# Kernel tuning notes

Hardware: AMD Instinct MI355X
Metric: run time of the kernel (lower is better)

Reference implementation:

```python
import jax, jax.numpy as jnp
import numpy as np

B, N, CIN, H, OUT, L, K = 8, 512, 64, 64, 64, 256, 3
EPS = 1e-5


def setup_inputs() -> dict:
    key = jax.random.key(0)
    ks = jax.random.split(key, 12)
    def unif(k, shape, fan):
        s = 1.0 / np.sqrt(fan)
        return jax.random.uniform(k, shape, jnp.float32, -s, s)
    return {
        "x": jax.random.normal(ks[0], (B, N, CIN, L), jnp.float32),
        "adj": jax.random.uniform(ks[1], (B, N, N), jnp.float32),
        # temp_conv1: Conv1d(CIN->H, k=3)
        "w1": unif(ks[2], (H, CIN, K), CIN * K),
        "b1": unif(ks[3], (H,), CIN * K),
        # graph_conv: Linear-style (H,H) + bias, stdv=1/sqrt(out_features)
        "gw": unif(ks[4], (H, H), H),
        "gb": unif(ks[5], (H,), H),
        # temp_conv2: Conv1d(H->OUT, k=3)
        "w2": unif(ks[6], (OUT, H, K), H * K),
        "b2": unif(ks[7], (OUT,), H * K),
        # residual: Conv1d(CIN->OUT, k=1) == pointwise linear
        "wr": unif(ks[8], (OUT, CIN), CIN),
        "br": unif(ks[9], (OUT,), CIN),
        # BatchNorm2d(OUT) affine params
        "gamma": jnp.ones((OUT,), jnp.float32),
        "beta": jnp.zeros((OUT,), jnp.float32),
    }


def _conv1d(x, w, b, pad):
    # x: (B, N, C, L) -> flatten node dim into batch, NCH conv
    b_, n_, c, l = x.shape
    y = jax.lax.conv_general_dilated(
        x.reshape(b_ * n_, c, l), w, window_strides=(1,),
        padding=[(pad, pad)], dimension_numbers=("NCH", "OIH", "NCH"))
    y = y + b[None, :, None]
    return y.reshape(b_, n_, w.shape[0], l)


def reference(x, adj, w1, b1, gw, gb, w2, b2, wr, br, gamma, beta):
    pad = (K - 1) // 2
    # residual branch: 1x1 conv over channels
    residual = jnp.einsum("bncl,oc->bnol", x, wr) + br[None, None, :, None]
    # temporal conv 1
    out = _conv1d(x, w1, b1, pad)                      # (B,N,H,L)
    # graph conv over all timesteps at once (replaces per-t Python loop)
    xw = jnp.einsum("bnhl,hd->bndl", out, gw)          # (B,N,H,L)
    out = jnp.einsum("bnm,bmdl->bndl", adj, xw) + gb[None, None, :, None]
    # temporal conv 2
    out = _conv1d(out, w2, b2, pad)                    # (B,N,OUT,L)
    out = out + residual
    # BatchNorm2d over channel axis (training-mode batch stats, biased var)
    mean = jnp.mean(out, axis=(0, 1, 3), keepdims=True)
    var = jnp.mean(jnp.square(out - mean), axis=(0, 1, 3), keepdims=True)
    out = (out - mean) * jax.lax.rsqrt(var + EPS)
    out = out * gamma[None, None, :, None] + beta[None, None, :, None]
    return jax.nn.relu(out)
```

## Files before the change

### kernel.cpp

```cpp
#include <hip/hip_runtime.h>
#include <hip/hip_bf16.h>
#include <stdint.h>


typedef unsigned short u16;
typedef unsigned int   u32;
typedef __attribute__((ext_vector_type(8))) short           bf16x8;
typedef __attribute__((ext_vector_type(8))) unsigned short  u16x8;
typedef __attribute__((ext_vector_type(4))) unsigned short  u16x4;
typedef __attribute__((ext_vector_type(4))) float           f32x4;

__device__ __forceinline__ float bf2f(u16 v){
  union { u32 u; float f; } x; x.u = ((u32)v) << 16; return x.f;
}
__device__ __forceinline__ u16 f2bf(float f){
  __hip_bfloat16 h = __float2bfloat16(f);
  return *reinterpret_cast<u16*>(&h);
}
__device__ __forceinline__ u32 swz(int row, int cbyte){
  return (u32)(row * 128) + (u32)(cbyte ^ ((row & 7) << 4));
}

__global__ __launch_bounds__(256) void k_prep(const float* __restrict__ w1, const float* __restrict__ b1,
    const float* __restrict__ gw, const float* __restrict__ w2, const float* __restrict__ wr,
    u16* __restrict__ w1g, float* __restrict__ b1g, u16* __restrict__ w2t, u16* __restrict__ wrt){
  const int gt = blockIdx.x * 256 + threadIdx.x, gs = gridDim.x * 256;
  for (int e = gt; e < 12288; e += gs){
    int tap = e >> 12, rem = e & 4095, o = rem >> 6, c = rem & 63;
    w2t[e] = f2bf(w2[(o * 64 + c) * 3 + tap]);
    float s = 0.f;
    for (int h = 0; h < 64; ++h)
      s += gw[h * 64 + o] * w1[(h * 64 + c) * 3 + tap];
    w1g[e] = f2bf(s);
  }
  for (int e = gt; e < 4096; e += gs) wrt[e] = f2bf(wr[e]);
  for (int d = gt; d < 64; d += gs){
    float s = 0.f;
    for (int h = 0; h < 64; ++h) s += b1[h] * gw[h * 64 + d];
    b1g[d] = s;
  }
}

__global__ __launch_bounds__(256) void k_p1(const float* __restrict__ x,
    const u16* __restrict__ w1g, const float* __restrict__ b1g,
    const u16* __restrict__ wrt, u16* __restrict__ outA, u16* __restrict__ outR){
  __shared__ u16 tile[16384];
  const int t = threadIdx.x;
  const size_t bn = (size_t)blockIdx.x + (size_t)blockIdx.y * 512;
  const float* xb = x + bn * 16384;

  {
    const int c0 = (t >> 3) * 2;
    #pragma unroll
    for (int v = 0; v < 8; ++v){
      const int l0 = (t & 7) * 4 + v * 32;
      f32x4 a = *(const f32x4*)(xb + (size_t)c0 * 256 + l0);
      f32x4 b = *(const f32x4*)(xb + (size_t)(c0 + 1) * 256 + l0);
      #pragma unroll
      for (int e = 0; e < 4; ++e){
        u32 p = (u32)f2bf(a[e]) | ((u32)f2bf(b[e]) << 16);
        *(u32*)((char*)tile + swz(l0 + e, c0 * 2)) = p;
      }
    }
  }
  __syncthreads();
  const int w = t >> 6, ln = t & 63, lq = ln >> 4, lr = ln & 15;
  const bf16x8 z8 = {};

  {
    f32x4 racc[4][4];
    #pragma unroll
    for (int i = 0; i < 4; ++i)
      #pragma unroll
      for (int j = 0; j < 4; ++j) racc[i][j] = (f32x4){0.f, 0.f, 0.f, 0.f};
    #pragma unroll
    for (int kk = 0; kk < 2; ++kk){
      bf16x8 A[4];
      #pragma unroll
      for (int fo = 0; fo < 4; ++fo)
        A[fo] = *(const bf16x8*)(wrt + (fo * 16 + lr) * 64 + kk * 32 + lq * 8);
      #pragma unroll
      for (int fc = 0; fc < 4; ++fc){
        int l = w * 64 + fc * 16 + lr;
        bf16x8 B = *(const bf16x8*)((char*)tile + swz(l, kk * 64 + lq * 16));
        #pragma unroll
        for (int fo = 0; fo < 4; ++fo)
          racc[fo][fc] = __builtin_amdgcn_mfma_f32_16x16x32_bf16(A[fo], B, racc[fo][fc], 0, 0, 0);
      }
    }
    #pragma unroll
    for (int v = 0; v < 8; ++v){
      u16x8 ov;
      const int fo = v >> 1;
      #pragma unroll
      for (int h = 0; h < 2; ++h){
        const int fc = (v & 1) * 2 + h;
        #pragma unroll
        for (int r2 = 0; r2 < 4; ++r2)
          ov[h * 4 + r2] = f2bf(racc[fo][fc][r2]);
      }
      *(u16x8*)(outR + bn * 16384 + v * 2048 + t * 8) = ov;
    }
  }

  f32x4 acc[4][4];
  #pragma unroll
  for (int i = 0; i < 4; ++i)
    #pragma unroll
    for (int j = 0; j < 4; ++j) acc[i][j] = (f32x4){0.f, 0.f, 0.f, 0.f};
  #pragma unroll
  for (int tap = 0; tap < 3; ++tap){
    #pragma unroll
    for (int kk = 0; kk < 2; ++kk){
      bf16x8 A[4];
      #pragma unroll
      for (int fo = 0; fo < 4; ++fo)
        A[fo] = *(const bf16x8*)(w1g + tap * 4096 + (fo * 16 + lr) * 64 + kk * 32 + lq * 8);
      #pragma unroll
      for (int fc = 0; fc < 4; ++fc){
        int r = w * 64 + fc * 16 + lr + tap - 1;
        int rc = r < 0 ? 0 : (r > 255 ? 255 : r);
        bf16x8 B = *(const bf16x8*)((char*)tile + swz(rc, kk * 64 + lq * 16));
        if (r != rc) B = z8;
        #pragma unroll
        for (int fo = 0; fo < 4; ++fo)
          acc[fo][fc] = __builtin_amdgcn_mfma_f32_16x16x32_bf16(A[fo], B, acc[fo][fc], 0, 0, 0);
      }
    }
  }
  __syncthreads();
  #pragma unroll
  for (int fo = 0; fo < 4; ++fo){
    float bb[4];
    #pragma unroll
    for (int r2 = 0; r2 < 4; ++r2) bb[r2] = b1g[fo * 16 + lq * 4 + r2];
    #pragma unroll
    for (int fc = 0; fc < 4; ++fc){
      int l = w * 64 + fc * 16 + lr;
      #pragma unroll
      for (int r2 = 0; r2 < 4; ++r2){
        int d = fo * 16 + lq * 4 + r2;
        *(u16*)((char*)tile + l * 128 + ((2 * d) ^ ((l & 7) << 4))) = f2bf(acc[fo][fc][r2] + bb[r2]);
      }
    }
  }
  __syncthreads();
  u16* op = outA + bn * 16384;
  #pragma unroll
  for (int v = 0; v < 8; ++v){
    int flat = v * 2048 + t * 8;
    int l = flat >> 6, d0 = flat & 63;
    u16x8 val = *(const u16x8*)((char*)tile + l * 128 + ((d0 * 2) ^ ((l & 7) << 4)));
    *(u16x8*)(op + flat) = val;
  }
}

__global__ __launch_bounds__(256) void k_p3(const u16* __restrict__ xw,
    const float* __restrict__ adj, const float* __restrict__ gbv, u16* __restrict__ outB){
  __shared__ u16 At[8192];
  __shared__ u16 Bt[8192];
  const int t = threadIdx.x;
  const int wg = ((blockIdx.x & 7) << 9) | ((int)blockIdx.x >> 3);
  const int jt = wg & 127, nt = (wg >> 7) & 3, b = wg >> 9;
  const float* adjb = adj + ((size_t)b * 512 + (size_t)nt * 128) * 512;
  const u16* Xb = xw + (size_t)b * 8388608 + (size_t)jt * 128;
  const int w = t >> 6, ln = t & 63, lq = ln >> 4, lr = ln & 15;
  const int wrow = w >> 1, wcol = w & 1;
  const int mpair = t & 31, jq = t >> 5;
  f32x4 acc[4][4];
  #pragma unroll
  for (int i = 0; i < 4; ++i)
    #pragma unroll
    for (int j = 0; j < 4; ++j) acc[i][j] = (f32x4){0.f, 0.f, 0.f, 0.f};

  f32x4 ra[8];
  u16x8 rb[4];
  auto LOADK = [&](int ks){
    #pragma unroll
    for (int it = 0; it < 8; ++it){
      int c = it * 256 + t;
      int row = c >> 4, mc = c & 15;
      ra[it] = *(const f32x4*)(adjb + (size_t)row * 512 + ks * 64 + mc * 4);
    }
    const u16* s0 = Xb + (size_t)(ks * 64 + mpair * 2) * 16384 + jq * 16;
    const u16* s1 = s0 + 16384;
    #pragma unroll
    for (int v2 = 0; v2 < 2; ++v2){
      rb[v2 * 2]     = *(const u16x8*)(s0 + v2 * 8);
      rb[v2 * 2 + 1] = *(const u16x8*)(s1 + v2 * 8);
    }
  };

  LOADK(0);
  for (int ks = 0; ks < 8; ++ks){
    #pragma unroll
    for (int it = 0; it < 8; ++it){
      int c = it * 256 + t;
      int row = c >> 4, mc = c & 15;
      u16x4 pk;
      #pragma unroll
      for (int e = 0; e < 4; ++e) pk[e] = f2bf(ra[it][e]);
      *(u16x4*)((char*)At + (u32)(row * 128) + (u32)((mc * 8) ^ ((row & 7) << 4))) = pk;
    }
    #pragma unroll
    for (int v2 = 0; v2 < 2; ++v2){
      #pragma unroll
      for (int e = 0; e < 8; ++e){
        u32 p = (u32)(u16)rb[v2 * 2][e] | ((u32)(u16)rb[v2 * 2 + 1][e] << 16);
        *(u32*)((char*)Bt + swz(jq * 16 + v2 * 8 + e, mpair * 4)) = p;
      }
    }
    __syncthreads();
    if (ks < 7) LOADK(ks + 1);
    #pragma unroll
    for (int kk = 0; kk < 2; ++kk){
      bf16x8 Af[4], Bf[4];
      #pragma unroll
      for (int f = 0; f < 4; ++f){
        int rA = wrow * 64 + f * 16 + lr;
        Af[f] = *(const bf16x8*)((char*)At + swz(rA, kk * 64 + lq * 16));
        int rB = wcol * 64 + f * 16 + lr;
        Bf[f] = *(const bf16x8*)((char*)Bt + swz(rB, kk * 64 + lq * 16));
      }
      #pragma unroll
      for (int fr = 0; fr < 4; ++fr)
        #pragma unroll
        for (int fc = 0; fc < 4; ++fc)
          acc[fr][fc] = __builtin_amdgcn_mfma_f32_16x16x32_bf16(Af[fr], Bf[fc], acc[fr][fc], 0, 0, 0);
    }
    __syncthreads();
  }
  float gbl[4];
  #pragma unroll
  for (int fc = 0; fc < 4; ++fc) gbl[fc] = gbv[fc * 16 + lr];
  u16* ob = outB + ((size_t)b * 512 + (size_t)nt * 128) * 16384 + (size_t)jt * 128;
  #pragma unroll
  for (int fr = 0; fr < 4; ++fr)
    #pragma unroll
    for (int fc = 0; fc < 4; ++fc)
      #pragma unroll
      for (int r2 = 0; r2 < 4; ++r2){
        int n_ = wrow * 64 + fr * 16 + lq * 4 + r2;
        int j_ = wcol * 64 + fc * 16 + lr;
        ob[(size_t)n_ * 16384 + j_] = f2bf(acc[fr][fc][r2] + gbl[fc]);
      }
}

__global__ __launch_bounds__(256) void k_p4(const u16* __restrict__ g,
    const u16* __restrict__ resv, const u16* __restrict__ w2t,
    const float* __restrict__ b2v, const float* __restrict__ brv,
    u16* __restrict__ outP, float* __restrict__ spart){
  __shared__ u16 lbuf[32768];
  __shared__ float sc2[512];
  const int t = threadIdx.x;
  const int w = t >> 6, ln = t & 63, lq = ln >> 4, lr = ln & 15;
  const int blk = blockIdx.x;
  const bf16x8 z8 = {};

  auto DMA = [&](int tile, int buf){
    const u16* gsrc = g + ((size_t)blk * 8 + tile) * 16384;
    #pragma unroll
    for (int i = 0; i < 8; ++i){
      const int row = w * 64 + i * 8 + (ln >> 3);
      const int c = ln & 7;
      const u16* src = gsrc + (size_t)row * 64 + (size_t)((c ^ (row & 7)) * 8);
      u16* dst = lbuf + buf * 16384 + w * 4096 + i * 512;
      __builtin_amdgcn_global_load_lds(
          (const __attribute__((address_space(1))) void*)src,
          (__attribute__((address_space(3))) void*)dst, 16, 0, 0);
    }
  };

  float bball[16];
  #pragma unroll
  for (int fo = 0; fo < 4; ++fo)
    #pragma unroll
    for (int r2 = 0; r2 < 4; ++r2){
      int o = fo * 16 + lq * 4 + r2;
      bball[fo * 4 + r2] = b2v[o] + brv[o];
    }
  float psum[16], psq[16];
  #pragma unroll
  for (int i = 0; i < 16; ++i){ psum[i] = 0.f; psq[i] = 0.f; }

  DMA(0, 0);
  for (int tt = 0; tt < 8; ++tt){
    const size_t bn = (size_t)blk * 8 + tt;
    u16* cur = lbuf + (tt & 1) * 16384;
    if (tt == 0) asm volatile("s_waitcnt vmcnt(0)" ::: "memory");
    else         asm volatile("s_waitcnt vmcnt(16)" ::: "memory");
    __builtin_amdgcn_sched_barrier(0);
    __builtin_amdgcn_s_barrier();
    __builtin_amdgcn_sched_barrier(0);
    if (tt < 7) DMA(tt + 1, (tt + 1) & 1);
    __builtin_amdgcn_sched_barrier(0);

    u16x8 rv[8];
    #pragma unroll
    for (int v = 0; v < 8; ++v) rv[v] = *(const u16x8*)(resv + bn * 16384 + v * 2048 + t * 8);

    f32x4 acc[4][4];
    #pragma unroll
    for (int i = 0; i < 4; ++i)
      #pragma unroll
      for (int j = 0; j < 4; ++j) acc[i][j] = (f32x4){0.f, 0.f, 0.f, 0.f};
    #pragma unroll
    for (int tap = 0; tap < 3; ++tap){
      #pragma unroll
      for (int kk = 0; kk < 2; ++kk){
        bf16x8 A[4];
        #pragma unroll
        for (int fo = 0; fo < 4; ++fo)
          A[fo] = *(const bf16x8*)(w2t + tap * 4096 + (fo * 16 + lr) * 64 + kk * 32 + lq * 8);
        #pragma unroll
        for (int fc = 0; fc < 4; ++fc){
          int r = w * 64 + fc * 16 + lr + tap - 1;
          int rc = r < 0 ? 0 : (r > 255 ? 255 : r);
          bf16x8 B = *(const bf16x8*)((char*)cur + swz(rc, kk * 64 + lq * 16));
          if (r != rc) B = z8;
          #pragma unroll
          for (int fo = 0; fo < 4; ++fo)
            acc[fo][fc] = __builtin_amdgcn_mfma_f32_16x16x32_bf16(A[fo], B, acc[fo][fc], 0, 0, 0);
        }
      }
    }
    __builtin_amdgcn_sched_barrier(0);
    asm volatile("s_waitcnt lgkmcnt(0)" ::: "memory");
    __builtin_amdgcn_sched_barrier(0);
    __builtin_amdgcn_s_barrier();
    __builtin_amdgcn_sched_barrier(0);
    #pragma unroll
    for (int fo = 0; fo < 4; ++fo){
      #pragma unroll
      for (int fc = 0; fc < 4; ++fc){
        int l = w * 64 + fc * 16 + lr;
        #pragma unroll
        for (int r2 = 0; r2 < 4; ++r2){
          float val = acc[fo][fc][r2] + bball[fo * 4 + r2]
                    + bf2f(rv[fo * 2 + (fc >> 1)][(fc & 1) * 4 + r2]);
          int o = fo * 16 + lq * 4 + r2;
          cur[o * 256 + (l ^ ((o & 7) * 8))] = f2bf(val);
          psum[fo * 4 + r2] += val;
          psq[fo * 4 + r2] += val * val;
        }
      }
    }
    __builtin_amdgcn_sched_barrier(0);
    asm volatile("s_waitcnt lgkmcnt(0)" ::: "memory");
    __builtin_amdgcn_sched_barrier(0);
    __builtin_amdgcn_s_barrier();
    __builtin_amdgcn_sched_barrier(0);
    u16* op = outP + bn * 16384;
    #pragma unroll
    for (int v = 0; v < 8; ++v){
      int d = (t >> 5) + v * 8;
      int l0 = (t & 31) * 8;
      u16x8 val = *(const u16x8*)(cur + d * 256 + (l0 ^ ((d & 7) * 8)));
      *(u16x8*)(op + v * 2048 + t * 8) = val;
    }
    __builtin_amdgcn_sched_barrier(0);
  }

  #pragma unroll
  for (int i = 0; i < 16; ++i){
    #pragma unroll
    for (int m = 1; m < 16; m <<= 1){
      psum[i] += __shfl_xor(psum[i], m, 64);
      psq[i]  += __shfl_xor(psq[i],  m, 64);
    }
  }
  if (lr == 0){
    #pragma unroll
    for (int i = 0; i < 16; ++i){
      int o = (i >> 2) * 16 + lq * 4 + (i & 3);
      sc2[w * 128 + o]      = psum[i];
      sc2[w * 128 + 64 + o] = psq[i];
    }
  }
  __syncthreads();
  if (t < 128){
    float tot = sc2[t] + sc2[128 + t] + sc2[256 + t] + sc2[384 + t];
    spart[(size_t)t * 512 + blk] = tot;
  }
}

__global__ __launch_bounds__(256) void k_p5(const float* __restrict__ part, float* __restrict__ fin){
  const int o = blockIdx.x, t = threadIdx.x;
  float s1 = 0.f, s2 = 0.f;
  for (int k = t; k < 512; k += 256){
    s1 += part[(size_t)o * 512 + k];
    s2 += part[(size_t)(64 + o) * 512 + k];
  }
  #pragma unroll
  for (int m = 32; m; m >>= 1){
    s1 += __shfl_down(s1, m, 64);
    s2 += __shfl_down(s2, m, 64);
  }
  __shared__ float red[8];
  if ((t & 63) == 0){ red[(t >> 6) * 2] = s1; red[(t >> 6) * 2 + 1] = s2; }
  __syncthreads();
  if (t == 0){
    float S1 = red[0] + red[2] + red[4] + red[6];
    float S2 = red[1] + red[3] + red[5] + red[7];
    const float invN = 1.f / 1048576.f;
    float mean = S1 * invN;
    float var = S2 * invN - mean * mean;
    fin[o] = mean;
    fin[64 + o] = rsqrtf(var + 1e-5f);
  }
}

__global__ __launch_bounds__(256) void k_p6(const u16* __restrict__ pre, const float* __restrict__ fin,
    const float* __restrict__ gamma, const float* __restrict__ beta, float* __restrict__ out){
  __shared__ float ssca[64], soff[64];
  const int tt = threadIdx.x;
  if (tt < 64){
    float sc = fin[64 + tt] * gamma[tt];
    ssca[tt] = sc;
    soff[tt] = beta[tt] - fin[tt] * sc;
  }
  __syncthreads();
  const size_t nchunk = 8388608;
  for (size_t i = (size_t)blockIdx.x * 256 + tt; i < nchunk; i += (size_t)gridDim.x * 256){
    int o = (int)((i >> 5) & 63);
    float sca = ssca[o], off = soff[o];
    u16x8 v = *(const u16x8*)(pre + i * 8);
    f32x4 oa, ob;
    #pragma unroll
    for (int e = 0; e < 4; ++e){
      float f0 = bf2f(v[e]) * sca + off;
      float f1 = bf2f(v[4 + e]) * sca + off;
      oa[e] = f0 > 0.f ? f0 : 0.f;
      ob[e] = f1 > 0.f ? f1 : 0.f;
    }
    *(f32x4*)(out + i * 8)     = oa;
    *(f32x4*)(out + i * 8 + 4) = ob;
  }
}

extern "C" void kernel_launch(void* const* d_in, const int* in_sizes, int n_in,
                              void* d_out, int out_size, void* d_ws, size_t ws_size,
                              hipStream_t stream){
  const float* x     = (const float*)d_in[0];
  const float* adj   = (const float*)d_in[1];
  const float* w1    = (const float*)d_in[2];
  const float* b1    = (const float*)d_in[3];
  const float* gw    = (const float*)d_in[4];
  const float* gb    = (const float*)d_in[5];
  const float* w2    = (const float*)d_in[6];
  const float* b2    = (const float*)d_in[7];
  const float* wr    = (const float*)d_in[8];
  const float* br    = (const float*)d_in[9];
  const float* gamma = (const float*)d_in[10];
  const float* beta  = (const float*)d_in[11];
  (void)in_sizes; (void)n_in; (void)out_size; (void)ws_size;

  char* ws = (char*)d_ws;
  u16*   bufA  = (u16*)ws;
  float* spart = (float*)(ws + 134217728);
  float* sfin  = (float*)(ws + 136314880);
  u16*   w1g   = (u16*)(ws + 136315392);
  float* b1g   = (float*)(ws + 136339968);
  u16*   w2t   = (u16*)(ws + 136348160);
  u16*   wrt   = (u16*)(ws + 136372736);
  u16*   gbuf  = (u16*)d_out;
  u16*   bufR  = (u16*)d_out + 67108864;

  k_prep<<<16, 256, 0, stream>>>(w1, b1, gw, w2, wr, w1g, b1g, w2t, wrt);
  k_p1<<<dim3(512, 8, 1), 256, 0, stream>>>(x, w1g, b1g, wrt, bufA, bufR);
  k_p3<<<4096, 256, 0, stream>>>(bufA, adj, gb, gbuf);
  k_p4<<<512, 256, 0, stream>>>(gbuf, bufR, w2t, b2, br, bufA, spart);
  k_p5<<<64, 256, 0, stream>>>(spart, sfin);
  k_p6<<<2048, 256, 0, stream>>>(bufA, sfin, gamma, beta, (float*)d_out);
}
```

Baseline: 541.3 us.

## Split k_p1 into single-wave blocks over 64-step time stripes with halo

k_p1 now launches 64-thread blocks. Each block handles one node and a 64-timestep stripe, loading a 72-row halo stripe into a 9 KB LDS buffer instead of a 32 KB whole-node tile. Each block is a single wave, so all __syncthreads and the boundary clamp/zero-select logic go away, and the smaller LDS footprint allows more resident blocks per CU. The cost is re-reading and re-converting 8 halo rows per stripe and four times as many blocks.

```diff
diff --git a/kernel.cpp b/kernel.cpp
--- a/kernel.cpp
+++ b/kernel.cpp
@@ -41,31 +41,44 @@
   }
 }
 
-__global__ __launch_bounds__(256) void k_p1(const float* __restrict__ x,
+__global__ __launch_bounds__(64) void k_p1(const float* __restrict__ x,
     const u16* __restrict__ w1g, const float* __restrict__ b1g,
     const u16* __restrict__ wrt, u16* __restrict__ outA, u16* __restrict__ outR){
-  __shared__ u16 tile[16384];
-  const int t = threadIdx.x;
-  const size_t bn = (size_t)blockIdx.x + (size_t)blockIdx.y * 512;
+  __shared__ u16 stripe[4608];
+  const int ln = threadIdx.x;
+  const int blk = blockIdx.x;
+  const size_t bn = (size_t)(blk >> 2);
+  const int q = blk & 3;
   const float* xb = x + bn * 16384;
+  const int lq = ln >> 4, lr = ln & 15;
+  char* sb = (char*)stripe;
 
   {
-    const int c0 = (t >> 3) * 2;
-    #pragma unroll
-    for (int v = 0; v < 8; ++v){
-      const int l0 = (t & 7) * 4 + v * 32;
-      f32x4 a = *(const f32x4*)(xb + (size_t)c0 * 256 + l0);
-      f32x4 b = *(const f32x4*)(xb + (size_t)(c0 + 1) * 256 + l0);
-      #pragma unroll
-      for (int e = 0; e < 4; ++e){
-        u32 p = (u32)f2bf(a[e]) | ((u32)f2bf(b[e]) << 16);
-        *(u32*)((char*)tile + swz(l0 + e, c0 * 2)) = p;
-      }
-    }
-  }
-  __syncthreads();
-  const int w = t >> 6, ln = t & 63, lq = ln >> 4, lr = ln & 15;
-  const bf16x8 z8 = {};
+    const int cp8 = ln >> 3;
+    const int lo = (ln & 7) * 4;
+    #pragma unroll
+    for (int cg = 0; cg < 4; ++cg){
+      const int c0 = cg * 16 + cp8 * 2;
+      #pragma unroll
+      for (int v = 0; v < 3; ++v){
+        const int rr0 = v * 32 + lo;
+        if (rr0 < 72){
+          const int gl0 = q * 64 - 4 + rr0;
+          const bool oob = (gl0 < 0) || (gl0 > 252);
+          f32x4 a = {0.f,0.f,0.f,0.f}, b = {0.f,0.f,0.f,0.f};
+          if (!oob){
+            a = *(const f32x4*)(xb + (size_t)c0 * 256 + gl0);
+            b = *(const f32x4*)(xb + (size_t)(c0 + 1) * 256 + gl0);
+          }
+          #pragma unroll
+          for (int e = 0; e < 4; ++e){
+            u32 p = oob ? 0u : ((u32)f2bf(a[e]) | ((u32)f2bf(b[e]) << 16));
+            *(u32*)(sb + swz(rr0 + e, c0 * 2)) = p;
+          }
+        }
+      }
+    }
+  }
 
   {
     f32x4 racc[4][4];
@@ -81,8 +94,7 @@
         A[fo] = *(const bf16x8*)(wrt + (fo * 16 + lr) * 64 + kk * 32 + lq * 8);
       #pragma unroll
       for (int fc = 0; fc < 4; ++fc){
-        int l = w * 64 + fc * 16 + lr;
-        bf16x8 B = *(const bf16x8*)((char*)tile + swz(l, kk * 64 + lq * 16));
+        bf16x8 B = *(const bf16x8*)(sb + swz(fc * 16 + lr + 4, kk * 64 + lq * 16));
         #pragma unroll
         for (int fo = 0; fo < 4; ++fo)
           racc[fo][fc] = __builtin_amdgcn_mfma_f32_16x16x32_bf16(A[fo], B, racc[fo][fc], 0, 0, 0);
@@ -99,7 +111,7 @@
         for (int r2 = 0; r2 < 4; ++r2)
           ov[h * 4 + r2] = f2bf(racc[fo][fc][r2]);
       }
-      *(u16x8*)(outR + bn * 16384 + v * 2048 + t * 8) = ov;
+      *(u16x8*)(outR + bn * 16384 + v * 2048 + (q * 64 + ln) * 8) = ov;
     }
   }
 
@@ -118,17 +130,13 @@
         A[fo] = *(const bf16x8*)(w1g + tap * 4096 + (fo * 16 + lr) * 64 + kk * 32 + lq * 8);
       #pragma unroll
       for (int fc = 0; fc < 4; ++fc){
-        int r = w * 64 + fc * 16 + lr + tap - 1;
-        int rc = r < 0 ? 0 : (r > 255 ? 255 : r);
-        bf16x8 B = *(const bf16x8*)((char*)tile + swz(rc, kk * 64 + lq * 16));
-        if (r != rc) B = z8;
+        bf16x8 B = *(const bf16x8*)(sb + swz(fc * 16 + lr + tap + 3, kk * 64 + lq * 16));
         #pragma unroll
         for (int fo = 0; fo < 4; ++fo)
           acc[fo][fc] = __builtin_amdgcn_mfma_f32_16x16x32_bf16(A[fo], B, acc[fo][fc], 0, 0, 0);
       }
     }
   }
-  __syncthreads();
   #pragma unroll
   for (int fo = 0; fo < 4; ++fo){
     float bb[4];
@@ -136,22 +144,21 @@
     for (int r2 = 0; r2 < 4; ++r2) bb[r2] = b1g[fo * 16 + lq * 4 + r2];
     #pragma unroll
     for (int fc = 0; fc < 4; ++fc){
-      int l = w * 64 + fc * 16 + lr;
+      const int ll = fc * 16 + lr;
       #pragma unroll
       for (int r2 = 0; r2 < 4; ++r2){
-        int d = fo * 16 + lq * 4 + r2;
-        *(u16*)((char*)tile + l * 128 + ((2 * d) ^ ((l & 7) << 4))) = f2bf(acc[fo][fc][r2] + bb[r2]);
-      }
-    }
-  }
-  __syncthreads();
+        const int d = fo * 16 + lq * 4 + r2;
+        *(u16*)(sb + ll * 128 + ((2 * d) ^ ((ll & 7) << 4))) = f2bf(acc[fo][fc][r2] + bb[r2]);
+      }
+    }
+  }
   u16* op = outA + bn * 16384;
   #pragma unroll
   for (int v = 0; v < 8; ++v){
-    int flat = v * 2048 + t * 8;
-    int l = flat >> 6, d0 = flat & 63;
-    u16x8 val = *(const u16x8*)((char*)tile + l * 128 + ((d0 * 2) ^ ((l & 7) << 4)));
-    *(u16x8*)(op + flat) = val;
+    const int ll = v * 8 + (ln >> 3);
+    const int d0 = (ln & 7) * 8;
+    u16x8 val = *(const u16x8*)(sb + ll * 128 + ((d0 * 2) ^ ((ll & 7) << 4)));
+    *(u16x8*)(op + (size_t)(q * 64 + ll) * 64 + d0) = val;
   }
 }
 
@@ -467,7 +474,7 @@
   u16*   bufR  = (u16*)d_out + 67108864;
 
   k_prep<<<16, 256, 0, stream>>>(w1, b1, gw, w2, wr, w1g, b1g, w2t, wrt);
-  k_p1<<<dim3(512, 8, 1), 256, 0, stream>>>(x, w1g, b1g, wrt, bufA, bufR);
+  k_p1<<<16384, 64, 0, stream>>>(x, w1g, b1g, wrt, bufA, bufR);
   k_p3<<<4096, 256, 0, stream>>>(bufA, adj, gb, gbuf);
   k_p4<<<512, 256, 0, stream>>>(gbuf, bufR, w2t, b2, br, bufA, spart);
   k_p5<<<64, 256, 0, stream>>>(spart, sfin);
```

Result: slower. 562.8 us (+4.0%).
